# Optimization experiments

Measured on AMD Instinct MI355X. Metric: run time of the kernel, lower is better.

Reference implementation:

```python
import jax, jax.numpy as jnp
import numpy as np

N_NODES = 100000
N_EDGES = 3200000
IN_DIM = 16
HID = 64


def setup_inputs() -> dict:
    key = jax.random.key(0)
    k_x, k_e, k_w1, k_w2 = jax.random.split(key, 4)
    x = jax.random.normal(k_x, (N_NODES, IN_DIM), dtype=jnp.float32)
    edge_index = jax.random.randint(k_e, (2, N_EDGES), 0, N_NODES, dtype=jnp.int64)
    # PyTorch Linear default init: U(-1/sqrt(fan_in), 1/sqrt(fan_in)); use scaled normal analog
    W1 = jax.random.normal(k_w1, (2 * IN_DIM, HID), dtype=jnp.float32) / np.sqrt(2 * IN_DIM)
    b1 = jnp.zeros((HID,), dtype=jnp.float32)
    W2 = jax.random.normal(k_w2, (HID, 1), dtype=jnp.float32) / np.sqrt(HID)
    b2 = jnp.zeros((1,), dtype=jnp.float32)
    return {"x": x, "edge_index": edge_index, "W1": W1, "b1": b1, "W2": W2, "b2": b2}


def reference(x, edge_index, W1, b1, W2, b2):
    row = edge_index[0]
    col = edge_index[1]
    bi = x[col]                      # [E, IN_DIM] gather of receiver features
    bo = x[row]                      # [E, IN_DIM] gather of sender features
    B = jnp.concatenate([bi, bo], axis=-1)  # [E, 2*IN_DIM]
    h = jnp.tanh(B @ W1 + b1)        # [E, HID]
    return jax.nn.sigmoid(h @ W2 + b2)  # [E, 1]
```

## Files before the change

kernel.cpp:

```cpp
#include <hip/hip_runtime.h>


typedef __attribute__((ext_vector_type(8)))  short bf16x8;
typedef __attribute__((ext_vector_type(4)))  float f32x4;
typedef __attribute__((ext_vector_type(16))) float f32x16;
typedef __attribute__((ext_vector_type(4)))  unsigned short u16x4;

#define LOG2E 1.4426950408889634f

__device__ __forceinline__ float asm_exp2(float x) {
    float r;
    asm("v_exp_f32 %0, %1" : "=v"(r) : "v"(x));
    return r;
}
__device__ __forceinline__ float asm_rcp(float x) {
    float r;
    asm("v_rcp_f32 %0, %1" : "=v"(r) : "v"(x));
    return r;
}

template <bool B> struct BC { static constexpr bool value = B; };

__device__ __forceinline__ unsigned short f2bf(float f) {
    unsigned u = __float_as_uint(f);
    u += 0x7fffu + ((u >> 16) & 1u);
    return (unsigned short)(u >> 16);
}

__global__ void prep(const float* __restrict__ x, unsigned short* __restrict__ xb, int n,
                     const unsigned* __restrict__ ei, int* __restrict__ flag) {
    if (blockIdx.x == 0 && threadIdx.x < 64) {
        unsigned v = ei[2 * threadIdx.x + 1];
        unsigned long long nz = __ballot(v != 0u);
        if (threadIdx.x == 0) flag[0] = (nz == 0ull) ? 1 : 0;
    }
    int i = (blockIdx.x * blockDim.x + threadIdx.x) * 4;
    if (i >= n) return;
    f32x4 v = *(const f32x4*)(x + i);
    u16x4 o;
    o[0] = f2bf(v[0]); o[1] = f2bf(v[1]); o[2] = f2bf(v[2]); o[3] = f2bf(v[3]);
    *(u16x4*)(xb + i) = o;
}

__global__ void detect_idx64(const unsigned* __restrict__ ei, int* __restrict__ flag) {
    unsigned v = ei[2 * threadIdx.x + 1];
    unsigned long long nz = __ballot(v != 0u);
    if (threadIdx.x == 0) flag[0] = (nz == 0ull) ? 1 : 0;
}

struct IdxPair { int c, r; };

template <bool USE_XB, bool EXACT>
__global__ void __launch_bounds__(256)
edge_mlp(const void* __restrict__ ei,
         const float* __restrict__ x,
         const unsigned short* __restrict__ xb,
         const float* __restrict__ W1,
         const float* __restrict__ b1,
         const float* __restrict__ W2,
         const float* __restrict__ b2,
         float* __restrict__ out,
         const int* __restrict__ flag,
         int E, int ntiles)
{
    __shared__ float2 tbl[64];

    const int lane = threadIdx.x & 63;
    const int l31  = lane & 31;
    const int g    = lane >> 5;
    const int gwave  = blockIdx.x * (blockDim.x >> 6) + (threadIdx.x >> 6);
    const int nwaves = gridDim.x * (blockDim.x >> 6);

    const int idx64 = flag ? flag[0] : 0;
    const float S = 2.0f * LOG2E;

    {
        int tid = threadIdx.x;
        if (tid < 64) {
            int tg = tid >> 5, tb = (tid >> 4) & 1, tj = tid & 15;
            int rowv = (tj & 3) + 8 * (tj >> 2) + 4 * tg;
            int h = 32 * tb + rowv;
            float2 cw;
            cw.x = exp2f(S * b1[h]);
            cw.y = -2.0f * W2[h];
            tbl[tid] = cw;
        }
    }

    bf16x8 w1f00, w1f01, w1f10, w1f11;
    {
        union { bf16x8 v; unsigned short u[8]; } t00, t01, t10, t11;
#pragma unroll
        for (int b = 0; b < 8; ++b) {
            int k0 = 8 * g + b;
            t00.u[b] = f2bf(S * W1[(k0)      * 64 + l31]);
            t01.u[b] = f2bf(S * W1[(16 + k0) * 64 + l31]);
            t10.u[b] = f2bf(S * W1[(k0)      * 64 + 32 + l31]);
            t11.u[b] = f2bf(S * W1[(16 + k0) * 64 + 32 + l31]);
        }
        w1f00 = t00.v; w1f01 = t01.v; w1f10 = t10.v; w1f11 = t11.v;
    }

    float pbase = 0.f;
#pragma unroll
    for (int j = 0; j < 16; ++j) {
        int rowv = (j & 3) + 8 * (j >> 2) + 4 * g;
        pbase += W2[rowv] + W2[32 + rowv];
    }
    const float bias2 = b2[0];

    __syncthreads();
    const float4* t4 = (const float4*)(&tbl[g * 32]);

    const char* xbb  = (const char*)xb;
    const char* outb = (char*)out;
    const unsigned g16 = (unsigned)g << 4;

    auto body = [&](auto bc) {
        constexpr bool IDX64 = decltype(bc)::value;
        const unsigned sh = IDX64 ? 3u : 2u;
        const char* eiR = (const char*)ei;
        const char* eiC = (const char*)ei + ((size_t)E << sh);

        auto load_idx = [&](int tt) -> IdxPair {
            int e = tt * 32 + l31;
            unsigned ec;
            if (EXACT) ec = (unsigned)e;
            else       ec = (unsigned)(e < E ? e : E - 1);
            unsigned off = ec << sh;
            IdxPair ip;
            ip.r = *(const int*)(eiR + off);
            ip.c = *(const int*)(eiC + off);
            return ip;
        };
        auto gather = [&](int node) -> bf16x8 {
            if (USE_XB) {
                unsigned off = ((unsigned)node << 5) + g16;
                return *(const bf16x8*)(xbb + off);
            } else {
                const float* px = x + (size_t)node * 16 + 8 * g;
                f32x4 v0 = *(const f32x4*)px;
                f32x4 v1 = *(const f32x4*)(px + 4);
                union { bf16x8 v; unsigned short u[8]; } t;
#pragma unroll
                for (int b = 0; b < 4; ++b) { t.u[b] = f2bf(v0[b]); t.u[b + 4] = f2bf(v1[b]); }
                return t.v;
            }
        };

        int t = gwave;
        if (t >= ntiles) return;
        IdxPair ic = load_idx(t);
        bf16x8 fc = gather(ic.c);
        bf16x8 fr = gather(ic.r);
        int tn = t + nwaves;
        IdxPair inx = load_idx(tn < ntiles ? tn : ntiles - 1);

        const f32x16 ZC = 0.0f;

        while (true) {
            bf16x8 fcn = gather(inx.c);
            bf16x8 frn = gather(inx.r);
            int tnn = tn + nwaves;
            IdxPair inn = load_idx(tnn < ntiles ? tnn : ntiles - 1);

            f32x16 acc0 = __builtin_amdgcn_mfma_f32_32x32x16_bf16(w1f00, fc, ZC, 0, 0, 0);
            acc0        = __builtin_amdgcn_mfma_f32_32x32x16_bf16(w1f01, fr, acc0, 0, 0, 0);
            f32x16 acc1 = __builtin_amdgcn_mfma_f32_32x32x16_bf16(w1f10, fc, ZC, 0, 0, 0);
            acc1        = __builtin_amdgcn_mfma_f32_32x32x16_bf16(w1f11, fr, acc1, 0, 0, 0);

            float p = pbase;
#pragma unroll
            for (int q = 0; q < 8; ++q) {
                const f32x16& A = (q < 4) ? acc0 : acc1;
                int k = (q & 3) * 4;
                float4 c01 = t4[2 * q];
                float4 c23 = t4[2 * q + 1];
                float E0 = asm_exp2(A[k]);
                float E1 = asm_exp2(A[k + 1]);
                float E2 = asm_exp2(A[k + 2]);
                float E3 = asm_exp2(A[k + 3]);
                float D0 = fmaf(c01.x, E0, 1.0f);
                float D1 = fmaf(c01.z, E1, 1.0f);
                float D2 = fmaf(c23.x, E2, 1.0f);
                float D3 = fmaf(c23.z, E3, 1.0f);
                float D01 = D0 * D1;
                float D23 = D2 * D3;
                float N01 = fmaf(c01.y, D1, c01.w * D0);
                float N23 = fmaf(c23.y, D3, c23.w * D2);
                float N   = fmaf(N01, D23, N23 * D01);
                float P   = D01 * D23;
                p = fmaf(N, asm_rcp(P), p);
            }
            p += __shfl_xor(p, 32);
            float z = p + bias2;
            float res = asm_rcp(1.0f + asm_exp2(-z * LOG2E));

            unsigned eoff = ((unsigned)(t * 32 + l31)) << 2;
            if (EXACT) {
                if (lane < 32) *(float*)(outb + eoff) = res;
            } else {
                if (lane < 32 && (t * 32 + l31) < E) *(float*)(outb + eoff) = res;
            }

            if (tn >= ntiles) break;
            t = tn; tn = tnn;
            inx = inn; fc = fcn; fr = frn;
        }
    };

    if (idx64) body(BC<true>{});
    else       body(BC<false>{});
}

extern "C" void kernel_launch(void* const* d_in, const int* in_sizes, int n_in,
                              void* d_out, int out_size, void* d_ws, size_t ws_size,
                              hipStream_t stream)
{
    const float* x  = (const float*)d_in[0];
    const void*  ei = d_in[1];
    const float* W1 = (const float*)d_in[2];
    const float* b1 = (const float*)d_in[3];
    const float* W2 = (const float*)d_in[4];
    const float* b2 = (const float*)d_in[5];
    float* out = (float*)d_out;

    const int E      = in_sizes[1] / 2;
    const int nx     = in_sizes[0];
    const int ntiles = (E + 31) / 32;
    const bool exact = (E % 32) == 0;

    int* flag = nullptr;
    unsigned short* xb = nullptr;
    bool use_xb = false;
    if (ws_size >= 4) flag = (int*)d_ws;
    if (ws_size >= 256 + (size_t)nx * 2) {
        xb = (unsigned short*)((char*)d_ws + 256);
        use_xb = true;
    }

    if (use_xb) {
        int nth = (nx + 3) / 4;
        prep<<<(nth + 255) / 256, 256, 0, stream>>>(x, xb, nx, (const unsigned*)ei, flag);
    } else if (flag) {
        detect_idx64<<<1, 64, 0, stream>>>((const unsigned*)ei, flag);
    }

    int blocks = 1250;
    if (ntiles < blocks * 4) blocks = (ntiles + 3) / 4;
    if (use_xb) {
        if (exact) edge_mlp<true , true ><<<blocks, 256, 0, stream>>>(ei, x, xb, W1, b1, W2, b2, out, flag, E, ntiles);
        else       edge_mlp<true , false><<<blocks, 256, 0, stream>>>(ei, x, xb, W1, b1, W2, b2, out, flag, E, ntiles);
    } else {
        if (exact) edge_mlp<false, true ><<<blocks, 256, 0, stream>>>(ei, x, xb, W1, b1, W2, b2, out, flag, E, ntiles);
        else       edge_mlp<false, false><<<blocks, 256, 0, stream>>>(ei, x, xb, W1, b1, W2, b2, out, flag, E, ntiles);
    }
}
```

Baseline: 62.64 us.

## Process two 32-edge tiles per wave iteration with register-cached tanh table

Adds a paired-tile kernel, used when E is a multiple of 64, that handles 64 edges per wave iteration with two independent MFMA chains. Each half-wave's partial sum is exchanged with one shuffle, so all 64 lanes write an output instead of only 32. The tanh/W2 coefficient table is loaded from LDS into registers once rather than reread every tile, and the grid shrinks to 768 blocks. The trade-off is higher register pressure from doubled in-flight gathers and accumulators, which may lower occupancy.

```diff
diff --git a/kernel.cpp b/kernel.cpp
--- a/kernel.cpp
+++ b/kernel.cpp
@@ -50,18 +50,18 @@
 
 struct IdxPair { int c, r; };
 
-template <bool USE_XB, bool EXACT>
+template <bool USE_XB>
 __global__ void __launch_bounds__(256)
-edge_mlp(const void* __restrict__ ei,
-         const float* __restrict__ x,
-         const unsigned short* __restrict__ xb,
-         const float* __restrict__ W1,
-         const float* __restrict__ b1,
-         const float* __restrict__ W2,
-         const float* __restrict__ b2,
-         float* __restrict__ out,
-         const int* __restrict__ flag,
-         int E, int ntiles)
+edge_mlp_pair(const void* __restrict__ ei,
+              const float* __restrict__ x,
+              const unsigned short* __restrict__ xb,
+              const float* __restrict__ W1,
+              const float* __restrict__ b1,
+              const float* __restrict__ W2,
+              const float* __restrict__ b2,
+              float* __restrict__ out,
+              const int* __restrict__ flag,
+              int E, int npairs)
 {
     __shared__ float2 tbl[64];
 
@@ -110,6 +110,187 @@
     const float bias2 = b2[0];
 
     __syncthreads();
+
+    float4 cc[16];
+    {
+        const float4* t4 = (const float4*)(&tbl[g * 32]);
+#pragma unroll
+        for (int j = 0; j < 16; ++j) cc[j] = t4[j];
+    }
+
+    const char* xbb  = (const char*)xb;
+    const char* outb = (char*)out;
+    const unsigned g16 = (unsigned)g << 4;
+
+    auto body = [&](auto bc) {
+        constexpr bool IDX64 = decltype(bc)::value;
+        const unsigned sh = IDX64 ? 3u : 2u;
+        const char* eiR = (const char*)ei;
+        const char* eiC = (const char*)ei + ((size_t)E << sh);
+
+        auto load_idx4 = [&](int pp, IdxPair& a, IdxPair& b) {
+            unsigned base  = (((unsigned)pp << 6) + (unsigned)l31) << sh;
+            unsigned baseB = base + (32u << sh);
+            a.r = *(const int*)(eiR + base);
+            a.c = *(const int*)(eiC + base);
+            b.r = *(const int*)(eiR + baseB);
+            b.c = *(const int*)(eiC + baseB);
+        };
+        auto gather = [&](int node) -> bf16x8 {
+            if (USE_XB) {
+                unsigned off = ((unsigned)node << 5) + g16;
+                return *(const bf16x8*)(xbb + off);
+            } else {
+                const float* px = x + (size_t)node * 16 + 8 * g;
+                f32x4 v0 = *(const f32x4*)px;
+                f32x4 v1 = *(const f32x4*)(px + 4);
+                union { bf16x8 v; unsigned short u[8]; } t;
+#pragma unroll
+                for (int b = 0; b < 4; ++b) { t.u[b] = f2bf(v0[b]); t.u[b + 4] = f2bf(v1[b]); }
+                return t.v;
+            }
+        };
+
+        auto quad = [&](const f32x16& A, int k, float4 c01, float4 c23, float& p) {
+            float E0 = asm_exp2(A[k]);
+            float E1 = asm_exp2(A[k + 1]);
+            float E2 = asm_exp2(A[k + 2]);
+            float E3 = asm_exp2(A[k + 3]);
+            float D0 = fmaf(c01.x, E0, 1.0f);
+            float D1 = fmaf(c01.z, E1, 1.0f);
+            float D2 = fmaf(c23.x, E2, 1.0f);
+            float D3 = fmaf(c23.z, E3, 1.0f);
+            float D01 = D0 * D1;
+            float D23 = D2 * D3;
+            float N01 = fmaf(c01.y, D1, c01.w * D0);
+            float N23 = fmaf(c23.y, D3, c23.w * D2);
+            float N   = fmaf(N01, D23, N23 * D01);
+            float P   = D01 * D23;
+            p = fmaf(N, asm_rcp(P), p);
+        };
+
+        int pp = gwave;
+        if (pp >= npairs) return;
+        IdxPair iA, iB;
+        load_idx4(pp, iA, iB);
+        bf16x8 fcA = gather(iA.c), frA = gather(iA.r);
+        bf16x8 fcB = gather(iB.c), frB = gather(iB.r);
+        int pn = pp + nwaves;
+        IdxPair iAn, iBn;
+        load_idx4(pn < npairs ? pn : npairs - 1, iAn, iBn);
+
+        const f32x16 ZC = 0.0f;
+
+        while (true) {
+            bf16x8 fcAn = gather(iAn.c), frAn = gather(iAn.r);
+            bf16x8 fcBn = gather(iBn.c), frBn = gather(iBn.r);
+            int pnn = pn + nwaves;
+            IdxPair iAnn, iBnn;
+            load_idx4(pnn < npairs ? pnn : npairs - 1, iAnn, iBnn);
+
+            float pA = pbase;
+            {
+                f32x16 a0 = __builtin_amdgcn_mfma_f32_32x32x16_bf16(w1f00, fcA, ZC, 0, 0, 0);
+                a0        = __builtin_amdgcn_mfma_f32_32x32x16_bf16(w1f01, frA, a0, 0, 0, 0);
+                f32x16 a1 = __builtin_amdgcn_mfma_f32_32x32x16_bf16(w1f10, fcA, ZC, 0, 0, 0);
+                a1        = __builtin_amdgcn_mfma_f32_32x32x16_bf16(w1f11, frA, a1, 0, 0, 0);
+#pragma unroll
+                for (int q = 0; q < 4; ++q) quad(a0, q * 4, cc[2 * q],     cc[2 * q + 1], pA);
+#pragma unroll
+                for (int q = 0; q < 4; ++q) quad(a1, q * 4, cc[8 + 2 * q], cc[9 + 2 * q], pA);
+            }
+            float pB = pbase;
+            {
+                f32x16 a0 = __builtin_amdgcn_mfma_f32_32x32x16_bf16(w1f00, fcB, ZC, 0, 0, 0);
+                a0        = __builtin_amdgcn_mfma_f32_32x32x16_bf16(w1f01, frB, a0, 0, 0, 0);
+                f32x16 a1 = __builtin_amdgcn_mfma_f32_32x32x16_bf16(w1f10, fcB, ZC, 0, 0, 0);
+                a1        = __builtin_amdgcn_mfma_f32_32x32x16_bf16(w1f11, frB, a1, 0, 0, 0);
+#pragma unroll
+                for (int q = 0; q < 4; ++q) quad(a0, q * 4, cc[2 * q],     cc[2 * q + 1], pB);
+#pragma unroll
+                for (int q = 0; q < 4; ++q) quad(a1, q * 4, cc[8 + 2 * q], cc[9 + 2 * q], pB);
+            }
+
+            float own   = g ? pB : pA;
+            float cross = g ? pA : pB;
+            own += __shfl_xor(cross, 32);
+            float z = own + bias2;
+            float res = asm_rcp(1.0f + asm_exp2(-z * LOG2E));
+
+            unsigned eoff = (((unsigned)pp << 6) + (unsigned)lane) << 2;
+            *(float*)(outb + eoff) = res;
+
+            if (pn >= npairs) break;
+            pp = pn; pn = pnn;
+            iAn = iAnn; iBn = iBnn;
+            fcA = fcAn; frA = frAn; fcB = fcBn; frB = frBn;
+        }
+    };
+
+    if (idx64) body(BC<true>{});
+    else       body(BC<false>{});
+}
+
+template <bool USE_XB, bool EXACT>
+__global__ void __launch_bounds__(256)
+edge_mlp1(const void* __restrict__ ei,
+          const float* __restrict__ x,
+          const unsigned short* __restrict__ xb,
+          const float* __restrict__ W1,
+          const float* __restrict__ b1,
+          const float* __restrict__ W2,
+          const float* __restrict__ b2,
+          float* __restrict__ out,
+          const int* __restrict__ flag,
+          int E, int ntiles)
+{
+    __shared__ float2 tbl[64];
+
+    const int lane = threadIdx.x & 63;
+    const int l31  = lane & 31;
+    const int g    = lane >> 5;
+    const int gwave  = blockIdx.x * (blockDim.x >> 6) + (threadIdx.x >> 6);
+    const int nwaves = gridDim.x * (blockDim.x >> 6);
+
+    const int idx64 = flag ? flag[0] : 0;
+    const float S = 2.0f * LOG2E;
+
+    {
+        int tid = threadIdx.x;
+        if (tid < 64) {
+            int tg = tid >> 5, tb = (tid >> 4) & 1, tj = tid & 15;
+            int rowv = (tj & 3) + 8 * (tj >> 2) + 4 * tg;
+            int h = 32 * tb + rowv;
+            float2 cw;
+            cw.x = exp2f(S * b1[h]);
+            cw.y = -2.0f * W2[h];
+            tbl[tid] = cw;
+        }
+    }
+
+    bf16x8 w1f00, w1f01, w1f10, w1f11;
+    {
+        union { bf16x8 v; unsigned short u[8]; } t00, t01, t10, t11;
+#pragma unroll
+        for (int b = 0; b < 8; ++b) {
+            int k0 = 8 * g + b;
+            t00.u[b] = f2bf(S * W1[(k0)      * 64 + l31]);
+            t01.u[b] = f2bf(S * W1[(16 + k0) * 64 + l31]);
+            t10.u[b] = f2bf(S * W1[(k0)      * 64 + 32 + l31]);
+            t11.u[b] = f2bf(S * W1[(16 + k0) * 64 + 32 + l31]);
+        }
+        w1f00 = t00.v; w1f01 = t01.v; w1f10 = t10.v; w1f11 = t11.v;
+    }
+
+    float pbase = 0.f;
+#pragma unroll
+    for (int j = 0; j < 16; ++j) {
+        int rowv = (j & 3) + 8 * (j >> 2) + 4 * g;
+        pbase += W2[rowv] + W2[32 + rowv];
+    }
+    const float bias2 = b2[0];
+
+    __syncthreads();
     const float4* t4 = (const float4*)(&tbl[g * 32]);
 
     const char* xbb  = (const char*)xb;
@@ -148,6 +329,24 @@
             }
         };
 
+        auto quad = [&](const f32x16& A, int k, float4 c01, float4 c23, float& p) {
+            float E0 = asm_exp2(A[k]);
+            float E1 = asm_exp2(A[k + 1]);
+            float E2 = asm_exp2(A[k + 2]);
+            float E3 = asm_exp2(A[k + 3]);
+            float D0 = fmaf(c01.x, E0, 1.0f);
+            float D1 = fmaf(c01.z, E1, 1.0f);
+            float D2 = fmaf(c23.x, E2, 1.0f);
+            float D3 = fmaf(c23.z, E3, 1.0f);
+            float D01 = D0 * D1;
+            float D23 = D2 * D3;
+            float N01 = fmaf(c01.y, D1, c01.w * D0);
+            float N23 = fmaf(c23.y, D3, c23.w * D2);
+            float N   = fmaf(N01, D23, N23 * D01);
+            float P   = D01 * D23;
+            p = fmaf(N, asm_rcp(P), p);
+        };
+
         int t = gwave;
         if (t >= ntiles) return;
         IdxPair ic = load_idx(t);
@@ -171,27 +370,10 @@
 
             float p = pbase;
 #pragma unroll
-            for (int q = 0; q < 8; ++q) {
-                const f32x16& A = (q < 4) ? acc0 : acc1;
-                int k = (q & 3) * 4;
-                float4 c01 = t4[2 * q];
-                float4 c23 = t4[2 * q + 1];
-                float E0 = asm_exp2(A[k]);
-                float E1 = asm_exp2(A[k + 1]);
-                float E2 = asm_exp2(A[k + 2]);
-                float E3 = asm_exp2(A[k + 3]);
-                float D0 = fmaf(c01.x, E0, 1.0f);
-                float D1 = fmaf(c01.z, E1, 1.0f);
-                float D2 = fmaf(c23.x, E2, 1.0f);
-                float D3 = fmaf(c23.z, E3, 1.0f);
-                float D01 = D0 * D1;
-                float D23 = D2 * D3;
-                float N01 = fmaf(c01.y, D1, c01.w * D0);
-                float N23 = fmaf(c23.y, D3, c23.w * D2);
-                float N   = fmaf(N01, D23, N23 * D01);
-                float P   = D01 * D23;
-                p = fmaf(N, asm_rcp(P), p);
-            }
+            for (int q = 0; q < 4; ++q) quad(acc0, q * 4, t4[2 * q],     t4[2 * q + 1], p);
+#pragma unroll
+            for (int q = 0; q < 4; ++q) quad(acc1, q * 4, t4[8 + 2 * q], t4[9 + 2 * q], p);
+
             p += __shfl_xor(p, 32);
             float z = p + bias2;
             float res = asm_rcp(1.0f + asm_exp2(-z * LOG2E));
@@ -228,7 +410,6 @@
     const int E      = in_sizes[1] / 2;
     const int nx     = in_sizes[0];
     const int ntiles = (E + 31) / 32;
-    const bool exact = (E % 32) == 0;
 
     int* flag = nullptr;
     unsigned short* xb = nullptr;
@@ -246,13 +427,26 @@
         detect_idx64<<<1, 64, 0, stream>>>((const unsigned*)ei, flag);
     }
 
-    int blocks = 1250;
-    if (ntiles < blocks * 4) blocks = (ntiles + 3) / 4;
-    if (use_xb) {
-        if (exact) edge_mlp<true , true ><<<blocks, 256, 0, stream>>>(ei, x, xb, W1, b1, W2, b2, out, flag, E, ntiles);
-        else       edge_mlp<true , false><<<blocks, 256, 0, stream>>>(ei, x, xb, W1, b1, W2, b2, out, flag, E, ntiles);
+    if ((E & 63) == 0) {
+        const int npairs = E / 64;
+        int blocks = 768;
+        if (npairs < blocks * 4) blocks = (npairs + 3) / 4;
+        if (blocks < 1) blocks = 1;
+        if (use_xb)
+            edge_mlp_pair<true ><<<blocks, 256, 0, stream>>>(ei, x, xb, W1, b1, W2, b2, out, flag, E, npairs);
+        else
+            edge_mlp_pair<false><<<blocks, 256, 0, stream>>>(ei, x, xb, W1, b1, W2, b2, out, flag, E, npairs);
     } else {
-        if (exact) edge_mlp<false, true ><<<blocks, 256, 0, stream>>>(ei, x, xb, W1, b1, W2, b2, out, flag, E, ntiles);
-        else       edge_mlp<false, false><<<blocks, 256, 0, stream>>>(ei, x, xb, W1, b1, W2, b2, out, flag, E, ntiles);
-    }
-}
+        const bool exact = (E % 32) == 0;
+        int blocks = 1250;
+        if (ntiles < blocks * 4) blocks = (ntiles + 3) / 4;
+        if (blocks < 1) blocks = 1;
+        if (use_xb) {
+            if (exact) edge_mlp1<true , true ><<<blocks, 256, 0, stream>>>(ei, x, xb, W1, b1, W2, b2, out, flag, E, ntiles);
+            else       edge_mlp1<true , false><<<blocks, 256, 0, stream>>>(ei, x, xb, W1, b1, W2, b2, out, flag, E, ntiles);
+        } else {
+            if (exact) edge_mlp1<false, true ><<<blocks, 256, 0, stream>>>(ei, x, xb, W1, b1, W2, b2, out, flag, E, ntiles);
+            else       edge_mlp1<false, false><<<blocks, 256, 0, stream>>>(ei, x, xb, W1, b1, W2, b2, out, flag, E, ntiles);
+        }
+    }
+}
```

New measurement: 60.35 us, median of 2. -3.7%, faster.
